# Optimization experiments

Measured on AMD Instinct MI355X. Metric: run time of the kernel, lower is better.

The kernel has to match this reference:

```python
import jax, jax.numpy as jnp
import numpy as np

D_MODEL = 2048
D_INNER = 2048
D_XB = 512
N_HEADS = 32
HEADDIM = 64   # P
DSTATE = 64    # N
N_KV = D_XB // DSTATE          # 8 kv heads
REP = N_HEADS // N_KV
D_FF = 8192
DCONV = 4
EPS = 1e-5
B, L = 1, 2048


def _rmsnorm(x, w, eps=EPS):
    return x * jax.lax.rsqrt(jnp.mean(x * x, axis=-1, keepdims=True) + eps) * w


def _silu(x):
    return x * jax.nn.sigmoid(x)


def _causal_dwconv(x, w, b):
    # x: (B,L,C), depthwise causal conv, kernel DCONV
    xp = jnp.pad(x, ((0, 0), (DCONV - 1, 0), (0, 0)))
    y = b
    for k in range(DCONV):  # small fixed kernel loop
        y = y + xp[:, k:k + x.shape[1], :] * w[:, k]
    return y


def setup_inputs() -> dict:
    key = jax.random.key(0)
    ks = jax.random.split(key, 10)
    s = 0.02
    d_proj = 2 * D_INNER + 2 * D_XB + N_HEADS  # z, x, B, C, dt
    conv_ch = 2 * D_XB + D_INNER               # conv over concat(x, B, C)
    return {
        "hidden_states": jax.random.normal(ks[0], (B, L, D_MODEL), jnp.float32),
        "in_proj_w": jax.random.normal(ks[1], (d_proj, D_MODEL), jnp.float32) * s,
        "conv_w": jax.random.normal(ks[2], (conv_ch, DCONV), jnp.float32) * s,
        "conv_b": jnp.zeros((conv_ch,), jnp.float32),
        "dt_bias": jax.random.normal(ks[3], (N_HEADS,), jnp.float32) * s,
        "A_log": jnp.log(jnp.arange(1, N_HEADS + 1, dtype=jnp.float32)),
        "D": jnp.ones((N_HEADS,), jnp.float32),
        "ssm_norm_w": jnp.ones((D_INNER,), jnp.float32),
        "out_proj_w": jax.random.normal(ks[4], (D_MODEL, D_INNER), jnp.float32) * s,
        "input_ln_w": jnp.ones((D_MODEL,), jnp.float32),
        "post_ln_w": jnp.ones((D_MODEL,), jnp.float32),
        "gate_w": jax.random.normal(ks[5], (D_FF, D_MODEL), jnp.float32) * s,
        "up_w": jax.random.normal(ks[6], (D_FF, D_MODEL), jnp.float32) * s,
        "down_w": jax.random.normal(ks[7], (D_MODEL, D_FF), jnp.float32) * s,
    }


def _mamba2(hs, in_proj_w, conv_w, conv_b, dt_bias, A_log, D, ssm_norm_w, out_proj_w):
    b, l, _ = hs.shape
    zxbcdt = hs @ in_proj_w.T
    z, x, Bm, Cm, dt = jnp.split(
        zxbcdt, [D_INNER, D_INNER + D_XB, D_INNER + 2 * D_XB, 2 * D_INNER + 2 * D_XB], axis=-1)
    # causal depthwise conv + silu over concat(x, B, C)
    xBC = _silu(_causal_dwconv(jnp.concatenate([x, Bm, Cm], axis=-1), conv_w, conv_b))
    x, Bm, Cm = jnp.split(xBC, [D_XB, 2 * D_XB], axis=-1)
    # heads (GQA: repeat x and B from N_KV to N_HEADS)
    x = jnp.repeat(x.reshape(b, l, N_KV, HEADDIM), REP, axis=2)      # (b,l,H,P)
    Bm = jnp.repeat(Bm.reshape(b, l, N_KV, DSTATE), REP, axis=2)     # (b,l,H,N)
    Cm = Cm.reshape(b, l, N_HEADS, DSTATE)                            # (b,l,H,N)
    dt = jax.nn.softplus(dt + dt_bias)                                # (b,l,H)
    dA = jnp.exp(dt * (-jnp.exp(A_log)))                              # (b,l,H)
    # selective scan over time
    xs = (jnp.moveaxis(dA, 1, 0), jnp.moveaxis(dt, 1, 0),
          jnp.moveaxis(x, 1, 0), jnp.moveaxis(Bm, 1, 0), jnp.moveaxis(Cm, 1, 0))
    h0 = jnp.zeros((b, N_HEADS, HEADDIM, DSTATE), hs.dtype)

    def step(h, t):
        dA_t, dt_t, x_t, B_t, C_t = t
        h = h * dA_t[:, :, None, None] + jnp.einsum('bh,bhp,bhn->bhpn', dt_t, x_t, B_t)
        y = jnp.einsum('bhpn,bhn->bhp', h, C_t)
        return h, y

    _, ys = jax.lax.scan(step, h0, xs)            # (l,b,H,P)
    y = jnp.moveaxis(ys, 0, 1) + D[None, None, :, None] * x
    y = y.reshape(b, l, D_INNER)
    y = _rmsnorm(y * _silu(z), ssm_norm_w)        # gated RMSNorm
    return y @ out_proj_w.T


def reference(hidden_states, in_proj_w, conv_w, conv_b, dt_bias, A_log, D,
              ssm_norm_w, out_proj_w, input_ln_w, post_ln_w, gate_w, up_w, down_w):
    residual = hidden_states
    h = _rmsnorm(hidden_states, input_ln_w)
    h = residual + _mamba2(h, in_proj_w, conv_w, conv_b, dt_bias, A_log, D,
                           ssm_norm_w, out_proj_w)
    residual = h
    h = _rmsnorm(h, post_ln_w)
    h = (_silu(h @ gate_w.T) * (h @ up_w.T)) @ down_w.T
    return residual + h
```

## Files before the change

### kernel.cpp

```cpp
#include <hip/hip_runtime.h>

typedef unsigned short u16;
typedef unsigned int u32;
typedef float f32x4 __attribute__((ext_vector_type(4)));
typedef __bf16 bf16x8 __attribute__((ext_vector_type(8)));
typedef unsigned short u16x8 __attribute__((ext_vector_type(8)));

#define L_SEQ 2048
#define DMODEL 2048
#define DINNER 2048
#define DXB 512
#define NHEADS 32
#define DPROJ 5152
#define DPROJ_PAD 5376
#define CONVCH 3072
#define DFF 8192
#define NCHUNK 32
#define CHUNK 64

__device__ __forceinline__ float bf2f(u16 u) {
  union { unsigned int i; float f; } v; v.i = ((unsigned int)u) << 16; return v.f;
}
__device__ __forceinline__ u16 f2bf(float f) {
  union { float f; unsigned int i; } v; v.f = f;
  unsigned int u = v.i;
  u += 0x7FFFu + ((u >> 16) & 1u);
  return (u16)(u >> 16);
}
__device__ __forceinline__ float siluf(float x) { return x / (1.f + __expf(-x)); }

#define GL16(gsrc, ldst) \
  __builtin_amdgcn_global_load_lds((const __attribute__((address_space(1))) u32*)(gsrc), \
                                   (__attribute__((address_space(3))) u32*)(ldst), 16, 0, 0)
#define SBAR() __builtin_amdgcn_s_barrier()
#define SCHED0() __builtin_amdgcn_sched_barrier(0)
#define WAIT_LGKM0() do { asm volatile("s_waitcnt lgkmcnt(0)" ::: "memory"); SCHED0(); } while (0)
#define WAIT_VM4() asm volatile("s_waitcnt vmcnt(4)" ::: "memory")
#define WAIT_VM0() asm volatile("s_waitcnt vmcnt(0)" ::: "memory")

__global__ __launch_bounds__(256) void cvt_k(
    const float* __restrict__ s, u16* __restrict__ d, int n8)
{
  const int i = blockIdx.x * 256 + threadIdx.x;
  if (i >= n8) return;
  f32x4 a = *(const f32x4*)(s + (size_t)i * 8);
  f32x4 b = *(const f32x4*)(s + (size_t)i * 8 + 4);
  u16x8 o;
#pragma unroll
  for (int j = 0; j < 4; ++j) { o[j] = f2bf(a[j]); o[j + 4] = f2bf(b[j]); }
  *(u16x8*)(d + (size_t)i * 8) = o;
}

__global__ __launch_bounds__(256) void cvt_pad_k(
    const float* __restrict__ s, u16* __restrict__ d)
{
  const int i = blockIdx.x * 256 + threadIdx.x;
  const int row = (i * 8) >> 11;
  u16x8 o;
  if (row < DPROJ) {
    f32x4 a = *(const f32x4*)(s + (size_t)i * 8);
    f32x4 b = *(const f32x4*)(s + (size_t)i * 8 + 4);
#pragma unroll
    for (int j = 0; j < 4; ++j) { o[j] = f2bf(a[j]); o[j + 4] = f2bf(b[j]); }
  } else {
#pragma unroll
    for (int j = 0; j < 8; ++j) o[j] = 0;
  }
  *(u16x8*)(d + (size_t)i * 8) = o;
}

template<int MH, int NH>
__device__ __forceinline__ void mfma16(f32x4 (&acc)[8][4], const bf16x8 (&af)[4][2],
                                       const bf16x8 (&bf)[2][2]) {
#pragma unroll
  for (int m = 0; m < 4; ++m)
#pragma unroll
    for (int n = 0; n < 2; ++n)
#pragma unroll
      for (int s = 0; s < 2; ++s)
        acc[MH * 4 + m][NH * 2 + n] = __builtin_amdgcn_mfma_f32_16x16x32_bf16(
            af[m][s], bf[n][s], acc[MH * 4 + m][NH * 2 + n], 0, 0, 0);
}

template<int EPI, int SPLIT>
__global__ __launch_bounds__(512, 2) void gemm8(
    const u16* __restrict__ A, const u16* __restrict__ W,
    void* __restrict__ Cptr, const u16* __restrict__ gateB,
    const int N, const int K, const int gx)
{
  __shared__ u16 sm[65536];
  const int tid = threadIdx.x;
  const int wid = tid >> 6, ln = tid & 63;
  const int wm = wid >> 2, wn = wid & 3;

  const int nwg = gridDim.x;
  int wg = (int)blockIdx.x;
  wg = (wg & 7) * (nwg >> 3) + (wg >> 3);
  const int tilesPerZ = gx * 8;
  const int bz = wg / tilesPerZ;
  const int rem = wg - bz * tilesPerZ;
  const int by = rem / gx;
  const int bx = rem - by * gx;
  const int m0 = by << 8, n0 = bx << 8;
  const int NT = (K >> 6) / SPLIT;
  const int ktB = bz * NT;

  f32x4 acc[8][4];
#pragma unroll
  for (int i = 0; i < 8; ++i)
#pragma unroll
    for (int j = 0; j < 4; ++j) acc[i][j] = f32x4{0.f, 0.f, 0.f, 0.f};

  const int l8r = ln >> 3;
  const int schunk = (ln & 7) ^ l8r;
  const int lr16 = ln & 15;
  const int q4 = ln >> 4;
  const int swz = ln & 7;
  const int c0 = ((q4 ^ swz) << 3);

  auto stageA = [&](int buf, int kt, int h) {
#pragma unroll
    for (int g = 0; g < 2; ++g) {
      const int rr = (wid << 3) + l8r;
      const size_t grow = (size_t)(m0 + (g << 7) + (h << 6) + rr);
      const u16* src = A + grow * K + (size_t)((ktB + kt) << 6) + (schunk << 3);
      u16* dst = &sm[(buf << 15) + (((h << 7) + (g << 6) + (wid << 3)) << 6)];
      GL16(src, dst);
    }
  };
  auto stageB = [&](int buf, int kt, int h) {
#pragma unroll
    for (int g = 0; g < 2; ++g) {
      const int v = (g << 6) + (wid << 3) + l8r;
      const int grow = n0 + ((v >> 5) << 6) + (h << 5) + (v & 31);
      const u16* src = W + (size_t)grow * K + (size_t)((ktB + kt) << 6) + (schunk << 3);
      u16* dst = &sm[(buf << 15) + 16384 + (((h << 7) + (g << 6) + (wid << 3)) << 6)];
      GL16(src, dst);
    }
  };

  bf16x8 af[4][2], bf[2][2];
  auto loadA = [&](int buf, int mh) {
#pragma unroll
    for (int m = 0; m < 4; ++m) {
      const int lrA = (mh << 7) + (wm << 6) + (m << 4) + lr16;
      const u16* p = &sm[(buf << 15) + (lrA << 6)];
      af[m][0] = *(const bf16x8*)(p + c0);
      af[m][1] = *(const bf16x8*)(p + (c0 ^ 32));
    }
  };
  auto loadB = [&](int buf, int nh) {
#pragma unroll
    for (int n = 0; n < 2; ++n) {
      const int lrB = (nh << 7) + (wn << 5) + (n << 4) + lr16;
      const u16* p = &sm[(buf << 15) + 16384 + (lrB << 6)];
      bf[n][0] = *(const bf16x8*)(p + c0);
      bf[n][1] = *(const bf16x8*)(p + (c0 ^ 32));
    }
  };

  stageA(0, 0, 0); stageA(0, 0, 1); stageB(0, 0, 0); stageB(0, 0, 1);
  stageA(1, 1, 0); stageB(1, 1, 1);
  WAIT_VM4();
  SBAR();

  for (int kt = 0; kt < NT; kt += 2) {
    const bool s2 = (kt + 2) < NT, s3 = (kt + 3) < NT;
    loadA(0, 0); loadB(0, 0);
    stageA(1, kt + 1, 1);
    SBAR(); WAIT_LGKM0();
    __builtin_amdgcn_s_setprio(1); mfma16<0, 0>(acc, af, bf); __builtin_amdgcn_s_setprio(0);
    SCHED0(); SBAR();
    loadB(0, 1);
    stageB(1, kt + 1, 0);
    SBAR(); WAIT_LGKM0();
    __builtin_amdgcn_s_setprio(1); mfma16<0, 1>(acc, af, bf); __builtin_amdgcn_s_setprio(0);
    SCHED0(); SBAR();
    loadA(0, 1);
    if (s2) stageA(0, kt + 2, 0);
    SBAR(); WAIT_LGKM0();
    __builtin_amdgcn_s_setprio(1); mfma16<1, 1>(acc, af, bf); __builtin_amdgcn_s_setprio(0);
    SCHED0(); SBAR();
    loadB(0, 0);
    if (s2) stageB(0, kt + 2, 1);
    SBAR(); WAIT_LGKM0();
    __builtin_amdgcn_s_setprio(1); mfma16<1, 0>(acc, af, bf); __builtin_amdgcn_s_setprio(0);
    SCHED0();
    if (s2) { WAIT_VM4(); } else { WAIT_VM0(); }
    SBAR();
    loadA(1, 0); loadB(1, 0);
    if (s2) stageA(0, kt + 2, 1);
    SBAR(); WAIT_LGKM0();
    __builtin_amdgcn_s_setprio(1); mfma16<0, 0>(acc, af, bf); __builtin_amdgcn_s_setprio(0);
    SCHED0(); SBAR();
    loadB(1, 1);
    if (s2) stageB(0, kt + 2, 0);
    SBAR(); WAIT_LGKM0();
    __builtin_amdgcn_s_setprio(1); mfma16<0, 1>(acc, af, bf); __builtin_amdgcn_s_setprio(0);
    SCHED0(); SBAR();
    loadA(1, 1);
    if (s3) stageA(1, kt + 3, 0);
    SBAR(); WAIT_LGKM0();
    __builtin_amdgcn_s_setprio(1); mfma16<1, 1>(acc, af, bf); __builtin_amdgcn_s_setprio(0);
    SCHED0(); SBAR();
    loadB(1, 0);
    if (s3) stageB(1, kt + 3, 1);
    SBAR(); WAIT_LGKM0();
    __builtin_amdgcn_s_setprio(1); mfma16<1, 0>(acc, af, bf); __builtin_amdgcn_s_setprio(0);
    SCHED0();
    if (s2) { if (s3) { WAIT_VM4(); } else { WAIT_VM0(); } }
    SBAR();
  }

  const int crow0 = m0 + (wm << 7) + (q4 << 2);
  const int ccol0 = n0 + (wn << 6) + lr16;
#pragma unroll
  for (int M = 0; M < 8; ++M) {
#pragma unroll
    for (int n = 0; n < 4; ++n) {
      const int col = ccol0 + (n << 4);
      if (col < N) {
#pragma unroll
        for (int j = 0; j < 4; ++j) {
          const size_t idx = (size_t)(crow0 + (M << 4) + j) * N + col;
          if (EPI == 0) {
            ((u16*)Cptr)[idx] = f2bf(acc[M][n][j]);
          } else if (EPI == 2) {
            float* P = (float*)Cptr + (size_t)bz * ((size_t)L_SEQ * N);
            P[idx] = acc[M][n][j];
          } else {
            ((u16*)Cptr)[idx] = f2bf(siluf(bf2f(gateB[idx])) * acc[M][n][j]);
          }
        }
      }
    }
  }
}

__global__ __launch_bounds__(256) void rmsnorm_k(
    const float* __restrict__ in, const float* __restrict__ w, u16* __restrict__ out)
{
  const int row = blockIdx.x, tid = threadIdx.x;
  const float* r = in + (size_t)row * DMODEL + tid * 8;
  f32x4 v0 = *(const f32x4*)r;
  f32x4 v1 = *(const f32x4*)(r + 4);
  float ss = v0[0]*v0[0] + v0[1]*v0[1] + v0[2]*v0[2] + v0[3]*v0[3]
           + v1[0]*v1[0] + v1[1]*v1[1] + v1[2]*v1[2] + v1[3]*v1[3];
#pragma unroll
  for (int off = 1; off < 64; off <<= 1) ss += __shfl_xor(ss, off);
  __shared__ float part[4];
  if ((tid & 63) == 0) part[tid >> 6] = ss;
  __syncthreads();
  const float tot = part[0] + part[1] + part[2] + part[3];
  const float scale = rsqrtf(tot * (1.f / DMODEL) + 1e-5f);
  f32x4 w0 = *(const f32x4*)(w + tid * 8);
  f32x4 w1 = *(const f32x4*)(w + tid * 8 + 4);
  u16x8 o;
#pragma unroll
  for (int j = 0; j < 4; ++j) {
    o[j]     = f2bf(v0[j] * scale * w0[j]);
    o[j + 4] = f2bf(v1[j] * scale * w1[j]);
  }
  *(u16x8*)(out + (size_t)row * DMODEL + tid * 8) = o;
}

__global__ __launch_bounds__(256) void red4_rms_k(
    const float* __restrict__ P, const float* __restrict__ resid,
    float* __restrict__ hres, const float* __restrict__ w, u16* __restrict__ h2)
{
  const int row = blockIdx.x, tid = threadIdx.x;
  const size_t base = (size_t)row * DMODEL + tid * 8;
  const size_t stride = (size_t)L_SEQ * DMODEL;
  f32x4 v0 = *(const f32x4*)(resid + base);
  f32x4 v1 = *(const f32x4*)(resid + base + 4);
#pragma unroll
  for (int p = 0; p < 4; ++p) {
    v0 += *(const f32x4*)(P + p * stride + base);
    v1 += *(const f32x4*)(P + p * stride + base + 4);
  }
  *(f32x4*)(hres + base) = v0;
  *(f32x4*)(hres + base + 4) = v1;
  float ss = v0[0]*v0[0] + v0[1]*v0[1] + v0[2]*v0[2] + v0[3]*v0[3]
           + v1[0]*v1[0] + v1[1]*v1[1] + v1[2]*v1[2] + v1[3]*v1[3];
#pragma unroll
  for (int off = 1; off < 64; off <<= 1) ss += __shfl_xor(ss, off);
  __shared__ float part[4];
  if ((tid & 63) == 0) part[tid >> 6] = ss;
  __syncthreads();
  const float tot = part[0] + part[1] + part[2] + part[3];
  const float scale = rsqrtf(tot * (1.f / DMODEL) + 1e-5f);
  f32x4 w0 = *(const f32x4*)(w + tid * 8);
  f32x4 w1 = *(const f32x4*)(w + tid * 8 + 4);
  u16x8 o;
#pragma unroll
  for (int j = 0; j < 4; ++j) {
    o[j]     = f2bf(v0[j] * scale * w0[j]);
    o[j + 4] = f2bf(v1[j] * scale * w1[j]);
  }
  *(u16x8*)(h2 + base) = o;
}

__global__ __launch_bounds__(256) void red4_add_k(
    const float* __restrict__ P, const float* __restrict__ resid, float* __restrict__ out)
{
  const size_t base = ((size_t)blockIdx.x * 256 + threadIdx.x) * 8;
  const size_t stride = (size_t)L_SEQ * DMODEL;
  f32x4 v0 = *(const f32x4*)(resid + base);
  f32x4 v1 = *(const f32x4*)(resid + base + 4);
#pragma unroll
  for (int p = 0; p < 4; ++p) {
    v0 += *(const f32x4*)(P + p * stride + base);
    v1 += *(const f32x4*)(P + p * stride + base + 4);
  }
  *(f32x4*)(out + base) = v0;
  *(f32x4*)(out + base + 4) = v1;
}

__global__ __launch_bounds__(256) void gated_rms_k(
    const float* __restrict__ y, const u16* __restrict__ zx,
    const float* __restrict__ w, u16* __restrict__ out)
{
  const int row = blockIdx.x, tid = threadIdx.x;
  const float* yr = y + (size_t)row * DINNER + tid * 8;
  f32x4 y0 = *(const f32x4*)yr;
  f32x4 y1 = *(const f32x4*)(yr + 4);
  u16x8 zv = *(const u16x8*)(zx + (size_t)row * DPROJ + tid * 8);
  float val[8];
#pragma unroll
  for (int j = 0; j < 4; ++j) {
    val[j]     = y0[j] * siluf(bf2f(zv[j]));
    val[j + 4] = y1[j] * siluf(bf2f(zv[j + 4]));
  }
  float ss = 0.f;
#pragma unroll
  for (int j = 0; j < 8; ++j) ss += val[j] * val[j];
#pragma unroll
  for (int off = 1; off < 64; off <<= 1) ss += __shfl_xor(ss, off);
  __shared__ float part[4];
  if ((tid & 63) == 0) part[tid >> 6] = ss;
  __syncthreads();
  const float tot = part[0] + part[1] + part[2] + part[3];
  const float scale = rsqrtf(tot * (1.f / DINNER) + 1e-5f);
  u16x8 o;
#pragma unroll
  for (int j = 0; j < 8; ++j) o[j] = f2bf(val[j] * scale * w[tid * 8 + j]);
  *(u16x8*)(out + (size_t)row * DINNER + tid * 8) = o;
}

__global__ __launch_bounds__(256) void conv_k(
    const u16* __restrict__ zx, const float* __restrict__ w,
    const float* __restrict__ b, u16* __restrict__ xbc)
{
  const int flat = blockIdx.x * 256 + threadIdx.x;
  const int t = flat / 384;
  const int c8 = (flat % 384) * 8;
  float acc[8];
  f32x4 b0 = *(const f32x4*)(b + c8);
  f32x4 b1 = *(const f32x4*)(b + c8 + 4);
#pragma unroll
  for (int j = 0; j < 4; ++j) { acc[j] = b0[j]; acc[j + 4] = b1[j]; }
  f32x4 wr[8];
#pragma unroll
  for (int j = 0; j < 8; ++j) wr[j] = *(const f32x4*)(w + (size_t)(c8 + j) * 4);
#pragma unroll
  for (int k = 0; k < 4; ++k) {
    const int tt = t - 3 + k;
    if (tt >= 0) {
      u16x8 xv = *(const u16x8*)(zx + (size_t)tt * DPROJ + DINNER + c8);
#pragma unroll
      for (int j = 0; j < 8; ++j) acc[j] += bf2f(xv[j]) * wr[j][k];
    }
  }
  u16x8 o;
#pragma unroll
  for (int j = 0; j < 8; ++j) o[j] = f2bf(siluf(acc[j]));
  *(u16x8*)(xbc + (size_t)t * CONVCH + c8) = o;
}

__global__ __launch_bounds__(256) void dt_k(
    const u16* __restrict__ zx, const float* __restrict__ dt_bias,
    const float* __restrict__ A_log, float* __restrict__ dtv, float* __restrict__ dAv)
{
  const int flat = blockIdx.x * 256 + threadIdx.x;
  const int t = flat >> 5, h = flat & 31;
  const float x = bf2f(zx[(size_t)t * DPROJ + (DPROJ - NHEADS) + h]) + dt_bias[h];
  const float sp = (x > 20.f) ? x : log1pf(expf(x));
  const float a = expf(A_log[h]);
  dtv[flat] = sp;
  dAv[flat] = expf(-a * sp);
}

__device__ __forceinline__ void stage16(float* dst, const u16* src) {
  u16x8 a = *(const u16x8*)src;
  u16x8 b = *(const u16x8*)(src + 8);
#pragma unroll
  for (int j = 0; j < 8; ++j) { dst[j] = bf2f(a[j]); dst[8 + j] = bf2f(b[j]); }
}

__global__ __launch_bounds__(256) void scan_a(
    const u16* __restrict__ xbc, const float* __restrict__ dtv,
    const float* __restrict__ dAv, const float* __restrict__ Dvec,
    float* __restrict__ y, float* __restrict__ S,
    float* __restrict__ gam, float* __restrict__ cum)
{
  __shared__ float xs[64][64], Bs[64][64], Cs[64][64];
  __shared__ float dts[64], dAs[64];
  const int c = blockIdx.x, h = blockIdx.y, kv = h >> 2;
  const int tid = threadIdx.x;
  const int t0 = c * CHUNK;
  {
    const int r = tid >> 2, cq = (tid & 3) * 16;
    const u16* base = xbc + (size_t)(t0 + r) * CONVCH;
    stage16(&xs[r][cq], base + kv * 64 + cq);
    stage16(&Bs[r][cq], base + DXB + kv * 64 + cq);
    stage16(&Cs[r][cq], base + 2 * DXB + h * 64 + cq);
    if (tid < 64) {
      dts[tid] = dtv[(size_t)(t0 + tid) * NHEADS + h];
      dAs[tid] = dAv[(size_t)(t0 + tid) * NHEADS + h];
    }
  }
  __syncthreads();
  const int p = tid >> 2, q = tid & 3;
  float hreg[16];
#pragma unroll
  for (int i = 0; i < 16; ++i) hreg[i] = 0.f;
  float cumv = 1.f;
  const float Dh = Dvec[h];
  for (int t = 0; t < CHUNK; ++t) {
    const float dtt = dts[t], dat = dAs[t];
    const float xv = xs[t][p];
    const float u = dtt * xv;
    float a0 = 0.f, a1 = 0.f, a2 = 0.f, a3 = 0.f;
#pragma unroll
    for (int i4 = 0; i4 < 4; ++i4) {
      f32x4 b4 = *(const f32x4*)&Bs[t][q * 16 + i4 * 4];
      f32x4 c4 = *(const f32x4*)&Cs[t][q * 16 + i4 * 4];
#pragma unroll
      for (int j = 0; j < 4; ++j) {
        const int i = i4 * 4 + j;
        hreg[i] = hreg[i] * dat + u * b4[j];
        if (i4 == 0) a0 += hreg[i] * c4[j];
        else if (i4 == 1) a1 += hreg[i] * c4[j];
        else if (i4 == 2) a2 += hreg[i] * c4[j];
        else a3 += hreg[i] * c4[j];
      }
    }
    float accv = (a0 + a1) + (a2 + a3);
    accv += __shfl_xor(accv, 1);
    accv += __shfl_xor(accv, 2);
    cumv *= dat;
    if (q == 0) y[(size_t)(t0 + t) * DINNER + h * 64 + p] = accv + Dh * xv;
    if (tid == 0) cum[(size_t)(t0 + t) * NHEADS + h] = cumv;
  }
  float* Sp = S + ((size_t)(c * NHEADS + h) << 12) + tid * 16;
#pragma unroll
  for (int i4 = 0; i4 < 4; ++i4)
    *(f32x4*)(Sp + i4 * 4) = f32x4{hreg[i4*4], hreg[i4*4+1], hreg[i4*4+2], hreg[i4*4+3]};
  if (tid == 0) gam[c * NHEADS + h] = cumv;
}

__global__ __launch_bounds__(256) void scan_b(
    const float* __restrict__ S, const float* __restrict__ gam, float* __restrict__ H)
{
  const int h = blockIdx.x, tid = threadIdx.x;
  float hr[16];
#pragma unroll
  for (int i = 0; i < 16; ++i) hr[i] = 0.f;
  for (int c = 0; c < NCHUNK; ++c) {
    const size_t base = ((size_t)(c * NHEADS + h) << 12) + tid * 16;
#pragma unroll
    for (int i4 = 0; i4 < 4; ++i4)
      *(f32x4*)(H + base + i4 * 4) = f32x4{hr[i4*4], hr[i4*4+1], hr[i4*4+2], hr[i4*4+3]};
    const float g = gam[c * NHEADS + h];
#pragma unroll
    for (int i4 = 0; i4 < 4; ++i4) {
      f32x4 s = *(const f32x4*)(S + base + i4 * 4);
#pragma unroll
      for (int j = 0; j < 4; ++j) hr[i4 * 4 + j] = g * hr[i4 * 4 + j] + s[j];
    }
  }
}

__global__ __launch_bounds__(256) void scan_c(
    const u16* __restrict__ xbc, const float* __restrict__ cum,
    const float* __restrict__ H, float* __restrict__ y)
{
  __shared__ float Cs[64][64];
  __shared__ float cums[64];
  const int c = blockIdx.x, h = blockIdx.y, tid = threadIdx.x;
  const int t0 = c * CHUNK;
  {
    const int r = tid >> 2, cq = (tid & 3) * 16;
    stage16(&Cs[r][cq], xbc + (size_t)(t0 + r) * CONVCH + 2 * DXB + h * 64 + cq);
    if (tid < 64) cums[tid] = cum[(size_t)(t0 + tid) * NHEADS + h];
  }
  const int p = tid >> 2, q = tid & 3;
  float hr[16];
  const size_t base = ((size_t)(c * NHEADS + h) << 12) + tid * 16;
#pragma unroll
  for (int i4 = 0; i4 < 4; ++i4) {
    f32x4 v = *(const f32x4*)(H + base + i4 * 4);
#pragma unroll
    for (int j = 0; j < 4; ++j) hr[i4 * 4 + j] = v[j];
  }
  __syncthreads();
  for (int t = 0; t < CHUNK; ++t) {
    float accv = 0.f;
#pragma unroll
    for (int i4 = 0; i4 < 4; ++i4) {
      f32x4 c4 = *(const f32x4*)&Cs[t][q * 16 + i4 * 4];
#pragma unroll
      for (int j = 0; j < 4; ++j) accv += hr[i4 * 4 + j] * c4[j];
    }
    accv += __shfl_xor(accv, 1);
    accv += __shfl_xor(accv, 2);
    if (q == 0) {
      const size_t idx = (size_t)(t0 + t) * DINNER + h * 64 + p;
      y[idx] += cums[t] * accv;
    }
  }
}

extern "C" void kernel_launch(void* const* d_in, const int* in_sizes, int n_in,
                              void* d_out, int out_size, void* d_ws, size_t ws_size,
                              hipStream_t stream) {
  const float* hs         = (const float*)d_in[0];
  const float* in_proj_w  = (const float*)d_in[1];
  const float* conv_w     = (const float*)d_in[2];
  const float* conv_b     = (const float*)d_in[3];
  const float* dt_bias    = (const float*)d_in[4];
  const float* A_log      = (const float*)d_in[5];
  const float* Dv         = (const float*)d_in[6];
  const float* ssm_w      = (const float*)d_in[7];
  const float* out_proj_w = (const float*)d_in[8];
  const float* in_ln_w    = (const float*)d_in[9];
  const float* post_ln_w  = (const float*)d_in[10];
  const float* gate_w     = (const float*)d_in[11];
  const float* up_w       = (const float*)d_in[12];
  const float* down_w     = (const float*)d_in[13];
  float* out = (float*)d_out;

  char* ws = (char*)d_ws;
  size_t off = 0;
  auto alloc = [&](size_t bytes) -> void* {
    void* p = ws + off;
    off = (off + bytes + 255) & ~(size_t)255;
    return p;
  };
  u16* wip = (u16*)alloc((size_t)DPROJ_PAD * DMODEL * 2);
  u16* wop = (u16*)alloc((size_t)DMODEL * DINNER * 2);
  u16* wg  = (u16*)alloc((size_t)DFF    * DMODEL * 2);
  u16* wu  = (u16*)alloc((size_t)DFF    * DMODEL * 2);
  u16* wd  = (u16*)alloc((size_t)DMODEL * DFF    * 2);
  u16*   zx  = (u16*)  alloc((size_t)L_SEQ * DPROJ * 2);
  u16*   xbc = (u16*)  alloc((size_t)L_SEQ * CONVCH * 2);
  float* Sv  = (float*)alloc((size_t)NCHUNK * NHEADS * 4096 * 4);
  float* Hv  = (float*)alloc((size_t)NCHUNK * NHEADS * 4096 * 4);
  float* pK  = (float*)zx;
  float* dtv = (float*)alloc((size_t)L_SEQ * NHEADS * 4);
  float* dAv = (float*)alloc((size_t)L_SEQ * NHEADS * 4);
  float* cum = (float*)alloc((size_t)L_SEQ * NHEADS * 4);
  float* gam = (float*)alloc((size_t)NCHUNK * NHEADS * 4);
  float* yv  = (float*)alloc((size_t)L_SEQ * DINNER * 4);
  float* hres= (float*)alloc((size_t)L_SEQ * DMODEL * 4);
  u16*  gateb= (u16*)  alloc((size_t)L_SEQ * DFF * 2);
  u16*  hslot= (u16*)  alloc((size_t)L_SEQ * DMODEL * 2);
  (void)ws_size; (void)in_sizes; (void)n_in; (void)out_size;

  cvt_pad_k<<<(DPROJ_PAD * DMODEL / 8) / 256, 256, 0, stream>>>(in_proj_w, wip);
  cvt_k<<<DMODEL * DINNER / 8 / 256, 256, 0, stream>>>(out_proj_w, wop, DMODEL * DINNER / 8);
  cvt_k<<<DFF * DMODEL / 8 / 256, 256, 0, stream>>>(gate_w, wg, DFF * DMODEL / 8);
  cvt_k<<<DFF * DMODEL / 8 / 256, 256, 0, stream>>>(up_w, wu, DFF * DMODEL / 8);
  cvt_k<<<DMODEL * DFF / 8 / 256, 256, 0, stream>>>(down_w, wd, DMODEL * DFF / 8);

  rmsnorm_k<<<L_SEQ, 256, 0, stream>>>(hs, in_ln_w, hslot);
  gemm8<0, 1><<<21 * 8, 512, 0, stream>>>(hslot, wip, zx, nullptr, DPROJ, DMODEL, 21);
  conv_k<<<(L_SEQ * (CONVCH / 8)) / 256, 256, 0, stream>>>(zx, conv_w, conv_b, xbc);
  dt_k<<<(L_SEQ * NHEADS) / 256, 256, 0, stream>>>(zx, dt_bias, A_log, dtv, dAv);
  scan_a<<<dim3(NCHUNK, NHEADS), 256, 0, stream>>>(xbc, dtv, dAv, Dv, yv, Sv, gam, cum);
  scan_b<<<NHEADS, 256, 0, stream>>>(Sv, gam, Hv);
  scan_c<<<dim3(NCHUNK, NHEADS), 256, 0, stream>>>(xbc, cum, Hv, yv);
  gated_rms_k<<<L_SEQ, 256, 0, stream>>>(yv, zx, ssm_w, hslot);
  gemm8<2, 4><<<8 * 8 * 4, 512, 0, stream>>>(hslot, wop, pK, nullptr, DMODEL, DINNER, 8);
  red4_rms_k<<<L_SEQ, 256, 0, stream>>>(pK, hs, hres, post_ln_w, hslot);
  gemm8<0, 1><<<32 * 8, 512, 0, stream>>>(hslot, wg, gateb, nullptr, DFF, DMODEL, 32);
  gemm8<3, 1><<<32 * 8, 512, 0, stream>>>(hslot, wu, gateb, gateb, DFF, DMODEL, 32);
  gemm8<2, 4><<<8 * 8 * 4, 512, 0, stream>>>(gateb, wd, pK, nullptr, DMODEL, DFF, 8);
  red4_add_k<<<(L_SEQ * DMODEL / 8) / 256, 256, 0, stream>>>(pK, hres, out);
}
```

Baseline: 538.6 us.

## Keep both B fragment halves in registers and remap tile order column-major

The B-operand fragments for both N halves are now held in separate registers (bfq[nh]), so the fourth MFMA phase in each k-step reuses the first B half instead of reloading it from LDS. This removes two LDS read phases per pair of k-steps, at the cost of extra VGPRs under a 512-thread, 2-block launch bound. The workgroup tile mapping also changes from row-major (by = rem/gx) to a fixed 8-row-major-in-M order (by = rem&7), which alters L2 reuse of weight and activation tiles. It also assumes exactly 8 M-tiles (L=2048 with 256-row tiles).

Result: no change. 531.4 us (-1.3%).

```diff
diff --git a/kernel.cpp b/kernel.cpp
--- a/kernel.cpp
+++ b/kernel.cpp
@@ -71,7 +71,7 @@
 
 template<int MH, int NH>
 __device__ __forceinline__ void mfma16(f32x4 (&acc)[8][4], const bf16x8 (&af)[4][2],
-                                       const bf16x8 (&bf)[2][2]) {
+                                       const bf16x8 (&bfq)[2][2][2]) {
 #pragma unroll
   for (int m = 0; m < 4; ++m)
 #pragma unroll
@@ -79,7 +79,7 @@
 #pragma unroll
       for (int s = 0; s < 2; ++s)
         acc[MH * 4 + m][NH * 2 + n] = __builtin_amdgcn_mfma_f32_16x16x32_bf16(
-            af[m][s], bf[n][s], acc[MH * 4 + m][NH * 2 + n], 0, 0, 0);
+            af[m][s], bfq[NH][n][s], acc[MH * 4 + m][NH * 2 + n], 0, 0, 0);
 }
 
 template<int EPI, int SPLIT>
@@ -96,11 +96,11 @@
   const int nwg = gridDim.x;
   int wg = (int)blockIdx.x;
   wg = (wg & 7) * (nwg >> 3) + (wg >> 3);
-  const int tilesPerZ = gx * 8;
+  const int tilesPerZ = gx << 3;
   const int bz = wg / tilesPerZ;
   const int rem = wg - bz * tilesPerZ;
-  const int by = rem / gx;
-  const int bx = rem - by * gx;
+  const int bx = rem >> 3;
+  const int by = rem & 7;
   const int m0 = by << 8, n0 = bx << 8;
   const int NT = (K >> 6) / SPLIT;
   const int ktB = bz * NT;
@@ -139,7 +139,7 @@
     }
   };
 
-  bf16x8 af[4][2], bf[2][2];
+  bf16x8 af[4][2], bfq[2][2][2];
   auto loadA = [&](int buf, int mh) {
 #pragma unroll
     for (int m = 0; m < 4; ++m) {
@@ -154,8 +154,8 @@
     for (int n = 0; n < 2; ++n) {
       const int lrB = (nh << 7) + (wn << 5) + (n << 4) + lr16;
       const u16* p = &sm[(buf << 15) + 16384 + (lrB << 6)];
-      bf[n][0] = *(const bf16x8*)(p + c0);
-      bf[n][1] = *(const bf16x8*)(p + (c0 ^ 32));
+      bfq[nh][n][0] = *(const bf16x8*)(p + c0);
+      bfq[nh][n][1] = *(const bf16x8*)(p + (c0 ^ 32));
     }
   };
 
@@ -169,44 +169,42 @@
     loadA(0, 0); loadB(0, 0);
     stageA(1, kt + 1, 1);
     SBAR(); WAIT_LGKM0();
-    __builtin_amdgcn_s_setprio(1); mfma16<0, 0>(acc, af, bf); __builtin_amdgcn_s_setprio(0);
+    __builtin_amdgcn_s_setprio(1); mfma16<0, 0>(acc, af, bfq); __builtin_amdgcn_s_setprio(0);
     SCHED0(); SBAR();
     loadB(0, 1);
     stageB(1, kt + 1, 0);
     SBAR(); WAIT_LGKM0();
-    __builtin_amdgcn_s_setprio(1); mfma16<0, 1>(acc, af, bf); __builtin_amdgcn_s_setprio(0);
+    __builtin_amdgcn_s_setprio(1); mfma16<0, 1>(acc, af, bfq); __builtin_amdgcn_s_setprio(0);
     SCHED0(); SBAR();
     loadA(0, 1);
     if (s2) stageA(0, kt + 2, 0);
     SBAR(); WAIT_LGKM0();
-    __builtin_amdgcn_s_setprio(1); mfma16<1, 1>(acc, af, bf); __builtin_amdgcn_s_setprio(0);
+    __builtin_amdgcn_s_setprio(1); mfma16<1, 1>(acc, af, bfq); __builtin_amdgcn_s_setprio(0);
     SCHED0(); SBAR();
-    loadB(0, 0);
     if (s2) stageB(0, kt + 2, 1);
     SBAR(); WAIT_LGKM0();
-    __builtin_amdgcn_s_setprio(1); mfma16<1, 0>(acc, af, bf); __builtin_amdgcn_s_setprio(0);
+    __builtin_amdgcn_s_setprio(1); mfma16<1, 0>(acc, af, bfq); __builtin_amdgcn_s_setprio(0);
     SCHED0();
     if (s2) { WAIT_VM4(); } else { WAIT_VM0(); }
     SBAR();
     loadA(1, 0); loadB(1, 0);
     if (s2) stageA(0, kt + 2, 1);
     SBAR(); WAIT_LGKM0();
-    __builtin_amdgcn_s_setprio(1); mfma16<0, 0>(acc, af, bf); __builtin_amdgcn_s_setprio(0);
+    __builtin_amdgcn_s_setprio(1); mfma16<0, 0>(acc, af, bfq); __builtin_amdgcn_s_setprio(0);
     SCHED0(); SBAR();
     loadB(1, 1);
     if (s2) stageB(0, kt + 2, 0);
     SBAR(); WAIT_LGKM0();
-    __builtin_amdgcn_s_setprio(1); mfma16<0, 1>(acc, af, bf); __builtin_amdgcn_s_setprio(0);
+    __builtin_amdgcn_s_setprio(1); mfma16<0, 1>(acc, af, bfq); __builtin_amdgcn_s_setprio(0);
     SCHED0(); SBAR();
     loadA(1, 1);
     if (s3) stageA(1, kt + 3, 0);
     SBAR(); WAIT_LGKM0();
-    __builtin_amdgcn_s_setprio(1); mfma16<1, 1>(acc, af, bf); __builtin_amdgcn_s_setprio(0);
+    __builtin_amdgcn_s_setprio(1); mfma16<1, 1>(acc, af, bfq); __builtin_amdgcn_s_setprio(0);
     SCHED0(); SBAR();
-    loadB(1, 0);
     if (s3) stageB(1, kt + 3, 1);
     SBAR(); WAIT_LGKM0();
-    __builtin_amdgcn_s_setprio(1); mfma16<1, 0>(acc, af, bf); __builtin_amdgcn_s_setprio(0);
+    __builtin_amdgcn_s_setprio(1); mfma16<1, 0>(acc, af, bfq); __builtin_amdgcn_s_setprio(0);
     SCHED0();
     if (s2) { if (s3) { WAIT_VM4(); } else { WAIT_VM0(); } }
     SBAR();
```
